# Performance work log

Hardware: AMD Instinct MI355X
Metric: run time of the kernel (lower is better)

The kernel has to match this reference:

```python
import jax, jax.numpy as jnp
import numpy as np

BATCH, GROUPS, ARITY, OUT_DIM = 1024, 512, 4, 64


def _high_order_act(X, params):
    # X: [B, G, K]; params: [G, 2**K, D]
    A_ind = jnp.argsort(X, axis=2)                                   # [B,G,K] int
    A_sort = jnp.take_along_axis(X, A_ind, axis=2)                   # sorted values
    # barycentric-style coefficients: smallest value, then successive gaps
    coef = jnp.concatenate(
        [A_sort[:, :, :1], A_sort[:, :, 1:] - A_sort[:, :, :-1]], axis=2
    )                                                                 # [B,G,K]
    # reversed cumulative sum of 2**A_ind -> vertex index into 2**K table
    pow2 = jnp.left_shift(jnp.int32(1), A_ind.astype(jnp.int32))      # [B,G,K]
    idx = jnp.flip(jnp.cumsum(jnp.flip(pow2, axis=2), axis=2), axis=2)  # [B,G,K]
    G = params.shape[0]
    g_idx = jnp.arange(G)[None, :, None]                              # [1,G,1]
    pg = params[g_idx, idx]                                           # [B,G,K,D] gather
    return jnp.einsum('bgk,bgkd->bgd', coef, pg)                      # [B,G,D]


def setup_inputs() -> dict:
    key = jax.random.key(0)
    k1, k2 = jax.random.split(key)
    X = jax.random.normal(k1, (BATCH, GROUPS, ARITY), dtype=jnp.float32)
    params = jax.random.normal(k2, (GROUPS, 2 ** ARITY, OUT_DIM), dtype=jnp.float32)
    return {"X": X, "params": params}


def reference(X, params):
    return _high_order_act(X, params)
```

## Files before the change

kernel.cpp:

```cpp
#include <hip/hip_runtime.h>

#define BATCH   1024
#define GROUPS  512
#define ARITY   4
#define OUT_DIM 64

__global__ __launch_bounds__(256) void hoact_kernel(
    const float4* __restrict__ X4,
    const float4* __restrict__ P4,
    float4*       __restrict__ O4)
{
    const int tid = blockIdx.x * blockDim.x + threadIdx.x;
    const int t   = tid & 7;
    const int bg  = tid >> 3;
    const int g   = bg & (GROUPS - 1);

    const float4 x = X4[bg];

    float v0 = __uint_as_float((__float_as_uint(x.x) & ~3u) | 0u);
    float v1 = __uint_as_float((__float_as_uint(x.y) & ~3u) | 1u);
    float v2 = __uint_as_float((__float_as_uint(x.z) & ~3u) | 2u);
    float v3 = __uint_as_float((__float_as_uint(x.w) & ~3u) | 3u);

#define CSWAP(a, b)                                  \
    {                                                \
        const float lo = fminf((a), (b));            \
        const float hi = fmaxf((a), (b));            \
        (a) = lo; (b) = hi;                          \
    }
    CSWAP(v0, v1);
    CSWAP(v2, v3);
    CSWAP(v0, v2);
    CSWAP(v1, v3);
    CSWAP(v1, v2);
#undef CSWAP

    const int i1 = __float_as_uint(v1) & 3;
    const int i2 = __float_as_uint(v2) & 3;
    const int i3 = __float_as_uint(v3) & 3;

    const float c0 = v0;
    const float c1 = v1 - v0;
    const float c2 = v2 - v1;
    const float c3 = v3 - v2;

    const int e3 = 1 << i3;
    const int e2 = e3 + (1 << i2);
    const int e1 = e2 + (1 << i1);

    const float4* base = P4 + (size_t)g * 256 + t;
    const float4 p0a = base[15 * 16];
    const float4 p0b = base[15 * 16 + 8];
    const float4 p1a = base[e1 * 16];
    const float4 p1b = base[e1 * 16 + 8];
    const float4 p2a = base[e2 * 16];
    const float4 p2b = base[e2 * 16 + 8];
    const float4 p3a = base[e3 * 16];
    const float4 p3b = base[e3 * 16 + 8];

    float4 oa, ob;
    oa.x = c0 * p0a.x + c1 * p1a.x + c2 * p2a.x + c3 * p3a.x;
    oa.y = c0 * p0a.y + c1 * p1a.y + c2 * p2a.y + c3 * p3a.y;
    oa.z = c0 * p0a.z + c1 * p1a.z + c2 * p2a.z + c3 * p3a.z;
    oa.w = c0 * p0a.w + c1 * p1a.w + c2 * p2a.w + c3 * p3a.w;
    ob.x = c0 * p0b.x + c1 * p1b.x + c2 * p2b.x + c3 * p3b.x;
    ob.y = c0 * p0b.y + c1 * p1b.y + c2 * p2b.y + c3 * p3b.y;
    ob.z = c0 * p0b.z + c1 * p1b.z + c2 * p2b.z + c3 * p3b.z;
    ob.w = c0 * p0b.w + c1 * p1b.w + c2 * p2b.w + c3 * p3b.w;

    O4[bg * 16 + t]     = oa;
    O4[bg * 16 + t + 8] = ob;
}

extern "C" void kernel_launch(void* const* d_in, const int* in_sizes, int n_in,
                              void* d_out, int out_size, void* d_ws, size_t ws_size,
                              hipStream_t stream) {
    const float4* X4 = (const float4*)d_in[0];
    const float4* P4 = (const float4*)d_in[1];
    float4*       O4 = (float4*)d_out;

    const int total_threads = BATCH * GROUPS * (OUT_DIM / 8);
    const int block = 256;
    const int grid  = total_threads / block;

    hipLaunchKernelGGL(hoact_kernel, dim3(grid), dim3(block), 0, stream,
                       X4, P4, O4);
}
```

Before: 163.3 us.

## Stage per-group param table in LDS and process 128 batch rows per block

Each block now owns one group and a chunk of 128 batch rows. It loads that group's 16x64 parameter table into padded shared memory once, then serves all four vertex gathers from LDS instead of global/L2. Each thread handles four batch rows, which adds per-thread work and a block barrier. Output and X accesses become strided across groups (512-float stride per batch row), which may hurt write coalescing compared with the previous contiguous mapping.

```diff
diff --git a/kernel.cpp b/kernel.cpp
--- a/kernel.cpp
+++ b/kernel.cpp
@@ -2,74 +2,99 @@
 
 #define BATCH   1024
 #define GROUPS  512
-#define ARITY   4
 #define OUT_DIM 64
+
+#define ROW_WORDS 68
 
 __global__ __launch_bounds__(256) void hoact_kernel(
     const float4* __restrict__ X4,
     const float4* __restrict__ P4,
     float4*       __restrict__ O4)
 {
-    const int tid = blockIdx.x * blockDim.x + threadIdx.x;
-    const int t   = tid & 7;
-    const int bg  = tid >> 3;
-    const int g   = bg & (GROUPS - 1);
+    __shared__ float tbl[16 * ROW_WORDS];
 
-    const float4 x = X4[bg];
+    const int g     = blockIdx.x >> 3;
+    const int chunk = blockIdx.x & 7;
+    const int b0    = chunk * 128;
+    const int tid   = threadIdx.x;
 
-    float v0 = __uint_as_float((__float_as_uint(x.x) & ~3u) | 0u);
-    float v1 = __uint_as_float((__float_as_uint(x.y) & ~3u) | 1u);
-    float v2 = __uint_as_float((__float_as_uint(x.z) & ~3u) | 2u);
-    float v3 = __uint_as_float((__float_as_uint(x.w) & ~3u) | 3u);
+    {
+        const float4 v = P4[g * 256 + tid];
+        const int row = tid >> 4, c4 = tid & 15;
+        *(float4*)&tbl[row * ROW_WORDS + c4 * 4] = v;
+    }
 
-#define CSWAP(a, b)                                  \
-    {                                                \
-        const float lo = fminf((a), (b));            \
-        const float hi = fmaxf((a), (b));            \
-        (a) = lo; (b) = hi;                          \
+    const int t       = tid & 7;
+    const int bl_base = tid >> 3;
+
+    float4 xv[4];
+#pragma unroll
+    for (int p = 0; p < 4; ++p) {
+        const int b = b0 + p * 32 + bl_base;
+        xv[p] = X4[b * GROUPS + g];
     }
-    CSWAP(v0, v1);
-    CSWAP(v2, v3);
-    CSWAP(v0, v2);
-    CSWAP(v1, v3);
-    CSWAP(v1, v2);
+
+    __syncthreads();
+
+#pragma unroll
+    for (int p = 0; p < 4; ++p) {
+        const int b = b0 + p * 32 + bl_base;
+        const float4 x = xv[p];
+
+        float v0 = __uint_as_float((__float_as_uint(x.x) & ~3u) | 0u);
+        float v1 = __uint_as_float((__float_as_uint(x.y) & ~3u) | 1u);
+        float v2 = __uint_as_float((__float_as_uint(x.z) & ~3u) | 2u);
+        float v3 = __uint_as_float((__float_as_uint(x.w) & ~3u) | 3u);
+
+#define CSWAP(a, b_)                                 \
+        {                                            \
+            const float lo = fminf((a), (b_));       \
+            const float hi = fmaxf((a), (b_));       \
+            (a) = lo; (b_) = hi;                     \
+        }
+        CSWAP(v0, v1);
+        CSWAP(v2, v3);
+        CSWAP(v0, v2);
+        CSWAP(v1, v3);
+        CSWAP(v1, v2);
 #undef CSWAP
 
-    const int i1 = __float_as_uint(v1) & 3;
-    const int i2 = __float_as_uint(v2) & 3;
-    const int i3 = __float_as_uint(v3) & 3;
+        const int i1 = __float_as_uint(v1) & 3;
+        const int i2 = __float_as_uint(v2) & 3;
+        const int i3 = __float_as_uint(v3) & 3;
 
-    const float c0 = v0;
-    const float c1 = v1 - v0;
-    const float c2 = v2 - v1;
-    const float c3 = v3 - v2;
+        const float c0 = v0;
+        const float c1 = v1 - v0;
+        const float c2 = v2 - v1;
+        const float c3 = v3 - v2;
 
-    const int e3 = 1 << i3;
-    const int e2 = e3 + (1 << i2);
-    const int e1 = e2 + (1 << i1);
+        const int e3 = 1 << i3;
+        const int e2 = e3 + (1 << i2);
+        const int e1 = e2 + (1 << i1);
 
-    const float4* base = P4 + (size_t)g * 256 + t;
-    const float4 p0a = base[15 * 16];
-    const float4 p0b = base[15 * 16 + 8];
-    const float4 p1a = base[e1 * 16];
-    const float4 p1b = base[e1 * 16 + 8];
-    const float4 p2a = base[e2 * 16];
-    const float4 p2b = base[e2 * 16 + 8];
-    const float4 p3a = base[e3 * 16];
-    const float4 p3b = base[e3 * 16 + 8];
+        const float4 p0a = *(const float4*)&tbl[15 * ROW_WORDS + t * 4];
+        const float4 p0b = *(const float4*)&tbl[15 * ROW_WORDS + (t + 8) * 4];
+        const float4 p1a = *(const float4*)&tbl[e1 * ROW_WORDS + t * 4];
+        const float4 p1b = *(const float4*)&tbl[e1 * ROW_WORDS + (t + 8) * 4];
+        const float4 p2a = *(const float4*)&tbl[e2 * ROW_WORDS + t * 4];
+        const float4 p2b = *(const float4*)&tbl[e2 * ROW_WORDS + (t + 8) * 4];
+        const float4 p3a = *(const float4*)&tbl[e3 * ROW_WORDS + t * 4];
+        const float4 p3b = *(const float4*)&tbl[e3 * ROW_WORDS + (t + 8) * 4];
 
-    float4 oa, ob;
-    oa.x = c0 * p0a.x + c1 * p1a.x + c2 * p2a.x + c3 * p3a.x;
-    oa.y = c0 * p0a.y + c1 * p1a.y + c2 * p2a.y + c3 * p3a.y;
-    oa.z = c0 * p0a.z + c1 * p1a.z + c2 * p2a.z + c3 * p3a.z;
-    oa.w = c0 * p0a.w + c1 * p1a.w + c2 * p2a.w + c3 * p3a.w;
-    ob.x = c0 * p0b.x + c1 * p1b.x + c2 * p2b.x + c3 * p3b.x;
-    ob.y = c0 * p0b.y + c1 * p1b.y + c2 * p2b.y + c3 * p3b.y;
-    ob.z = c0 * p0b.z + c1 * p1b.z + c2 * p2b.z + c3 * p3b.z;
-    ob.w = c0 * p0b.w + c1 * p1b.w + c2 * p2b.w + c3 * p3b.w;
+        float4 oa, ob;
+        oa.x = c0 * p0a.x + c1 * p1a.x + c2 * p2a.x + c3 * p3a.x;
+        oa.y = c0 * p0a.y + c1 * p1a.y + c2 * p2a.y + c3 * p3a.y;
+        oa.z = c0 * p0a.z + c1 * p1a.z + c2 * p2a.z + c3 * p3a.z;
+        oa.w = c0 * p0a.w + c1 * p1a.w + c2 * p2a.w + c3 * p3a.w;
+        ob.x = c0 * p0b.x + c1 * p1b.x + c2 * p2b.x + c3 * p3b.x;
+        ob.y = c0 * p0b.y + c1 * p1b.y + c2 * p2b.y + c3 * p3b.y;
+        ob.z = c0 * p0b.z + c1 * p1b.z + c2 * p2b.z + c3 * p3b.z;
+        ob.w = c0 * p0b.w + c1 * p1b.w + c2 * p2b.w + c3 * p3b.w;
 
-    O4[bg * 16 + t]     = oa;
-    O4[bg * 16 + t + 8] = ob;
+        const int o_idx = b * (GROUPS * 16) + g * 16 + t;
+        O4[o_idx]     = oa;
+        O4[o_idx + 8] = ob;
+    }
 }
 
 extern "C" void kernel_launch(void* const* d_in, const int* in_sizes, int n_in,
@@ -79,10 +104,7 @@
     const float4* P4 = (const float4*)d_in[1];
     float4*       O4 = (float4*)d_out;
 
-    const int total_threads = BATCH * GROUPS * (OUT_DIM / 8);
-    const int block = 256;
-    const int grid  = total_threads / block;
-
-    hipLaunchKernelGGL(hoact_kernel, dim3(grid), dim3(block), 0, stream,
+    const int grid = GROUPS * 8;
+    hipLaunchKernelGGL(hoact_kernel, dim3(grid), dim3(256), 0, stream,
                        X4, P4, O4);
 }
```

After: 145.3 us. 1.12x faster.
